# Kernel optimization log

Measured on AMD Instinct MI355X. Metric: run time of the kernel, lower is better.

## Reference

```python
import jax, jax.numpy as jnp
import numpy as np

S_MC = 4      # num_mc_samples
TEMP = 0.1    # soft_sampling temperature


def gcn_conv(x, adj, maskf, W, b):
    # DenseGCNConv: add self loops, sym-normalize, aggregate, linear, mask
    N = adj.shape[-1]
    A = adj + jnp.eye(N, dtype=adj.dtype)
    dis = jnp.clip(A.sum(-1), 1.0, None) ** -0.5
    A = dis[:, :, None] * A * dis[:, None, :]
    out = jnp.einsum('bij,bjf->bif', A, x @ W) + b
    return out * maskf[:, :, None]


def connected_components(adj, mask):
    # min-label propagation; labels in {1..N}, masked nodes -> 0
    B, N, _ = adj.shape
    labels0 = jnp.broadcast_to(jnp.arange(1, N + 1, dtype=jnp.int32), (B, N))
    big = jnp.int32(N + 2)
    adj_b = adj > 0
    def step(labels, _):
        nb = jnp.where(adj_b, labels[:, None, :], big)  # [B,N,N]
        return jnp.minimum(labels, nb.min(-1)), None
    labels, _ = jax.lax.scan(step, labels0, None, length=N)
    return jnp.where(mask, labels, 0)


def setup_inputs() -> dict:
    key = jax.random.key(0)
    ks = jax.random.split(key, 8)
    B, N, Fin, H, K = 512, 64, 128, 256, 32
    x = jax.random.normal(ks[0], (B, N, Fin), jnp.float32)
    lengths = jax.random.randint(ks[1], (B,), N // 2, N + 1)
    mask = jnp.arange(N)[None, :] < lengths[:, None]
    a = jax.random.uniform(ks[2], (B, N, N)) < 0.08
    adj = jnp.triu(a, 1)
    adj = (adj | jnp.swapaxes(adj, 1, 2)).astype(jnp.float32)
    adj = adj * mask[:, :, None] * mask[:, None, :]
    W1 = jax.random.normal(ks[3], (Fin, H), jnp.float32) / np.float32(np.sqrt(Fin))
    b1 = jnp.zeros((H,), jnp.float32)
    W2 = jax.random.normal(ks[4], (H, H), jnp.float32) / np.float32(np.sqrt(H))
    b2 = jnp.zeros((H,), jnp.float32)
    centroids = jax.random.normal(ks[5], (K, H), jnp.float32)
    return {'x': x, 'adj': adj, 'mask': mask, 'W1': W1, 'b1': b1, 'W2': W2, 'b2': b2, 'centroids': centroids}


def reference(x, adj, mask, W1, b1, W2, b2, centroids):
    B, N = mask.shape
    maskf = mask.astype(x.dtype)
    adj = adj * maskf[:, :, None] * maskf[:, None, :]
    # embedding convs
    h = jax.nn.relu(gcn_conv(x, adj, maskf, W1, b1))
    h = jax.nn.relu(gcn_conv(h, adj, maskf, W2, b2))
    # cdist to (detached) centroids, expanded form to avoid [B,N,K,F] blowup
    c = jax.lax.stop_gradient(centroids)
    d2 = (jnp.sum(h * h, -1, keepdims=True) + jnp.sum(c * c, -1)[None, None]
          - 2.0 * jnp.einsum('bnf,kf->bnk', h, c))
    dist = jnp.sqrt(jnp.clip(d2, 1e-12, None))  # [B,N,K]
    # softmin over clusters with temperature
    logits = -dist / TEMP
    probs = jax.nn.softmax(logits, -1)
    logp = jax.nn.log_softmax(logits, -1)
    # Categorical MC sampling via Gumbel-max
    g = jax.random.gumbel(jax.random.key(42), (S_MC,) + logp.shape, logp.dtype)
    concepts = jnp.argmax(logp[None] + g, -1).reshape(S_MC * B, N)  # [SB,N]
    # per-node sampled probability, product over valid nodes per graph (scatter mul)
    probs_r = jnp.tile(probs, (S_MC, 1, 1))
    node_p = jnp.take_along_axis(probs_r, concepts[..., None], -1)[..., 0]
    mask_r = jnp.tile(mask, (S_MC, 1))
    graph_prob = jnp.prod(jnp.where(mask_r, jax.lax.stop_gradient(node_p), 1.0), -1)  # [SB]
    # same-concept restricted adjacency -> connected components (undirected)
    adj_r = jnp.tile(adj, (S_MC, 1, 1))
    same = concepts[:, :, None] == concepts[:, None, :]
    adj_cc = jnp.where(same, adj_r, 0.0)
    adj_cc = jnp.maximum(adj_cc, jnp.swapaxes(adj_cc, 1, 2))
    labels = connected_components(adj_cc, mask_r)  # [SB,N], 0 reserved for masked
    # scatter-mean node embeddings per cluster; drop reserved cluster 0
    P = jax.nn.one_hot(labels, N + 1, dtype=x.dtype) * mask_r[..., None].astype(x.dtype)  # [SB,N,N+1]
    counts = P.sum(1)  # [SB,N+1]
    h_r = jnp.tile(h, (S_MC, 1, 1))
    new_x = (jnp.einsum('bnc,bnf->bcf', P, h_r) / jnp.clip(counts, 1.0, None)[..., None])[:, 1:, :]
    # pooled adjacency S^T A S, binarized
    new_adj = jnp.einsum('bic,bij,bjd->bcd', P, adj_r, P)[:, 1:, 1:]
    new_adj = (new_adj > 0).astype(x.dtype)
    return new_x, new_adj, graph_prob, labels
```

## Files before the change

kernel.cpp:

```cpp
#include <hip/hip_runtime.h>

#define B_    512

static constexpr float TINYF = 1.17549435e-38f;
typedef float fx4  __attribute__((ext_vector_type(4)));
typedef short bf16x8 __attribute__((ext_vector_type(8)));
typedef float f32x4 __attribute__((ext_vector_type(4)));
typedef unsigned short u16x4 __attribute__((ext_vector_type(4)));

__device__ __forceinline__ unsigned tf_bits(unsigned lo) {
  const unsigned ks0 = 0u, ks1 = 42u, ks2 = 0x1BD11BF0u;
  unsigned x0 = 0u + ks0;
  unsigned x1 = lo + ks1;
#define TFR(r) { x0 += x1; x1 = (x1 << r) | (x1 >> (32 - r)); x1 ^= x0; }
  TFR(13) TFR(15) TFR(26) TFR(6)
  x0 += ks1; x1 += ks2 + 1u;
  TFR(17) TFR(29) TFR(16) TFR(24)
  x0 += ks2; x1 += ks0 + 2u;
  TFR(13) TFR(15) TFR(26) TFR(6)
  x0 += ks0; x1 += ks1 + 3u;
  TFR(17) TFR(29) TFR(16) TFR(24)
  x0 += ks1; x1 += ks2 + 4u;
  TFR(13) TFR(15) TFR(26) TFR(6)
  x0 += ks2; x1 += ks0 + 5u;
#undef TFR
  return x0 ^ x1;
}

__device__ __forceinline__ void split3(float v, unsigned& b1, unsigned& b2, unsigned& b3) {
  unsigned u1 = __float_as_uint(v) & 0xFFFF0000u;
  float r1 = v - __uint_as_float(u1);
  unsigned u2 = __float_as_uint(r1) & 0xFFFF0000u;
  float r2 = r1 - __uint_as_float(u2);
  unsigned u3 = __float_as_uint(r2) & 0xFFFF0000u;
  b1 = u1 >> 16; b2 = u2 >> 16; b3 = u3 >> 16;
}

__device__ __forceinline__ unsigned short planeOf(float v, int s) {
  unsigned u1 = __float_as_uint(v) & 0xFFFF0000u;
  if (s == 0) return (unsigned short)(u1 >> 16);
  float r1 = v - __uint_as_float(u1);
  unsigned u2 = __float_as_uint(r1) & 0xFFFF0000u;
  if (s == 1) return (unsigned short)(u2 >> 16);
  float r2 = r1 - __uint_as_float(u2);
  return (unsigned short)((__float_as_uint(r2) & 0xFFFF0000u) >> 16);
}

#define MF6(A0, A1, A2, Bv0, Bv1, Bv2, ACC)                                   \
  ACC = __builtin_amdgcn_mfma_f32_16x16x32_bf16(A0, Bv0, ACC, 0, 0, 0);       \
  ACC = __builtin_amdgcn_mfma_f32_16x16x32_bf16(A0, Bv1, ACC, 0, 0, 0);       \
  ACC = __builtin_amdgcn_mfma_f32_16x16x32_bf16(A1, Bv0, ACC, 0, 0, 0);       \
  ACC = __builtin_amdgcn_mfma_f32_16x16x32_bf16(A0, Bv2, ACC, 0, 0, 0);       \
  ACC = __builtin_amdgcn_mfma_f32_16x16x32_bf16(A1, Bv1, ACC, 0, 0, 0);       \
  ACC = __builtin_amdgcn_mfma_f32_16x16x32_bf16(A2, Bv0, ACC, 0, 0, 0);

__global__ void k_setup(const float* __restrict__ W1, const float* __restrict__ W2,
                        const float* __restrict__ cen,
                        unsigned short* __restrict__ Wg1, unsigned short* __restrict__ Wg2,
                        unsigned short* __restrict__ cen3, float* __restrict__ ccbuf) {
  int bi = blockIdx.x, tid = threadIdx.x;
  if (bi < 144) {
    const float* W; unsigned short* Wg; int nk, s, ks, g;
    if (bi < 48) { W = W1; Wg = Wg1; nk = 4; s = bi >> 4; ks = (bi >> 2) & 3; g = bi & 3; }
    else { int t = bi - 48; W = W2; Wg = Wg2; nk = 8; s = t >> 5; ks = (t >> 2) & 7; g = t & 3; }
    int n = tid;
    bf16x8 hv;
#pragma unroll
    for (int jj = 0; jj < 8; ++jj) {
      float v = W[(size_t)(ks * 32 + g * 8 + jj) * 256 + n];
      hv[jj] = (short)planeOf(v, s);
    }
    *(bf16x8*)&Wg[((((size_t)s * nk + ks) * 4 + g) * 256 + n) * 8] = hv;
  } else if (bi == 144) {
    int k = tid >> 3, l8 = tid & 7;
    float s = 0.0f;
    for (int m = 0; m < 32; ++m) { float v = cen[k * 256 + l8 + 8 * m]; s += v * v; }
#pragma unroll
    for (int d = 1; d < 8; d <<= 1) s += __shfl_xor(s, d, 64);
    if (l8 == 0) ccbuf[k] = s;
  } else {
    int s = bi - 145;
    for (int u = 0; u < 4; ++u) {
      int idx = tid + 256 * u;
      int ks = idx >> 7, c = (idx >> 6) & 1, rem = idx & 63;
      int l15v = rem >> 2, lgv = rem & 3;
      bf16x8 hv;
#pragma unroll
      for (int jj = 0; jj < 8; ++jj)
        hv[jj] = (short)planeOf(cen[(size_t)(16 * c + l15v) * 256 + 32 * ks + 8 * lgv + jj], s);
      *(bf16x8*)&cen3[(size_t)s * 8192 + (size_t)idx * 8] = hv;
    }
  }
}

template<bool SRCL>
__device__ __forceinline__ void layer_core(const float* __restrict__ Aglob,
                                           const float (*hsrc)[260],
                                           float (*hdst)[260],
                                           const unsigned short* __restrict__ Wg, int nk,
                                           const unsigned short* AhP,
                                           const float* biaS, const float* maskS,
                                           char* U, int tid) {
  unsigned short (*Ap)[3][2112] = (unsigned short(*)[3][2112])U;
  unsigned short (*Tbuf)[72]    = (unsigned short(*)[72])U;
  int w = tid >> 6, l = tid & 63;
  int l15 = l & 15, lg = l >> 4;
  int K = nk * 32;
  int srow = tid >> 2, sg = tid & 3;
  const float* sp = SRCL ? (const float*)nullptr : (Aglob + (size_t)srow * K + sg * 8);

  {
    float vv[8];
    if (SRCL) {
      float4 v0 = *(const float4*)&hsrc[srow][sg * 8];
      float4 v1 = *(const float4*)&hsrc[srow][sg * 8 + 4];
      vv[0] = v0.x; vv[1] = v0.y; vv[2] = v0.z; vv[3] = v0.w;
      vv[4] = v1.x; vv[5] = v1.y; vv[6] = v1.z; vv[7] = v1.w;
    } else {
      float4 v0 = *(const float4*)(sp);
      float4 v1 = *(const float4*)(sp + 4);
      vv[0] = v0.x; vv[1] = v0.y; vv[2] = v0.z; vv[3] = v0.w;
      vv[4] = v1.x; vv[5] = v1.y; vv[6] = v1.z; vv[7] = v1.w;
    }
    bf16x8 p1, p2, p3;
#pragma unroll
    for (int jj = 0; jj < 8; ++jj) {
      unsigned h1, h2, h3; split3(vv[jj], h1, h2, h3);
      p1[jj] = (short)h1; p2[jj] = (short)h2; p3[jj] = (short)h3;
    }
    int off = sg * 528 + srow * 8;
    *(bf16x8*)&Ap[0][0][off] = p1;
    *(bf16x8*)&Ap[0][1][off] = p2;
    *(bf16x8*)&Ap[0][2][off] = p3;
  }
  __syncthreads();

  f32x4 acc1[4][4];
#pragma unroll
  for (int q = 0; q < 4; ++q)
#pragma unroll
    for (int c = 0; c < 4; ++c) acc1[q][c] = (f32x4){0.f, 0.f, 0.f, 0.f};

  const size_t wss = (size_t)nk * 8192;

  for (int ks = 0; ks < nk; ++ks) {
    int cur = ks & 1;
    float vv[8];
    bool pf = (ks + 1 < nk);
    if (pf) {
      if (SRCL) {
        float4 v0 = *(const float4*)&hsrc[srow][(ks + 1) * 32 + sg * 8];
        float4 v1 = *(const float4*)&hsrc[srow][(ks + 1) * 32 + sg * 8 + 4];
        vv[0] = v0.x; vv[1] = v0.y; vv[2] = v0.z; vv[3] = v0.w;
        vv[4] = v1.x; vv[5] = v1.y; vv[6] = v1.z; vv[7] = v1.w;
      } else {
        float4 v0 = *(const float4*)(sp + (ks + 1) * 32);
        float4 v1 = *(const float4*)(sp + (ks + 1) * 32 + 4);
        vv[0] = v0.x; vv[1] = v0.y; vv[2] = v0.z; vv[3] = v0.w;
        vv[4] = v1.x; vv[5] = v1.y; vv[6] = v1.z; vv[7] = v1.w;
      }
    }
    bf16x8 af[4][3];
#pragma unroll
    for (int q = 0; q < 4; ++q) {
      int off = lg * 528 + (16 * q + l15) * 8;
#pragma unroll
      for (int s = 0; s < 3; ++s) af[q][s] = *(const bf16x8*)&Ap[cur][s][off];
    }
#pragma unroll
    for (int c = 0; c < 4; ++c) {
      size_t wbase = (((size_t)ks * 4 + lg) * 256 + (64 * w + 16 * c + l15)) * 8;
      bf16x8 b0 = *(const bf16x8*)&Wg[wbase];
      bf16x8 b1 = *(const bf16x8*)&Wg[wbase + wss];
      bf16x8 b2 = *(const bf16x8*)&Wg[wbase + 2 * wss];
#pragma unroll
      for (int q = 0; q < 4; ++q) {
        MF6(af[q][0], af[q][1], af[q][2], b0, b1, b2, acc1[q][c]);
      }
    }
    if (pf) {
      bf16x8 p1, p2, p3;
#pragma unroll
      for (int jj = 0; jj < 8; ++jj) {
        unsigned h1, h2, h3; split3(vv[jj], h1, h2, h3);
        p1[jj] = (short)h1; p2[jj] = (short)h2; p3[jj] = (short)h3;
      }
      int off = sg * 528 + srow * 8;
      *(bf16x8*)&Ap[cur ^ 1][0][off] = p1;
      *(bf16x8*)&Ap[cur ^ 1][1][off] = p2;
      *(bf16x8*)&Ap[cur ^ 1][2][off] = p3;
    }
    __syncthreads();
  }

  f32x4 acc2[4][4];
#pragma unroll
  for (int q = 0; q < 4; ++q)
#pragma unroll
    for (int c = 0; c < 4; ++c) acc2[q][c] = (f32x4){0.f, 0.f, 0.f, 0.f};

#pragma unroll
  for (int sB = 0; sB < 3; ++sB) {
    const int nA = 3 - sB;
    __syncthreads();
#pragma unroll
    for (int q = 0; q < 4; ++q)
#pragma unroll
      for (int c = 0; c < 4; ++c) {
        u16x4 pv;
#pragma unroll
        for (int r = 0; r < 4; ++r) pv[r] = planeOf(acc1[q][c][r], sB);
        *(u16x4*)&Tbuf[64 * w + 16 * c + l15][16 * q + 4 * lg] = pv;
      }
    __syncthreads();
#pragma unroll
    for (int mt = 0; mt < 2; ++mt) {
      bf16x8 bf[4];
#pragma unroll
      for (int c = 0; c < 4; ++c)
        bf[c] = *(const bf16x8*)&Tbuf[64 * w + 16 * c + l15][32 * mt + 8 * lg];
#pragma unroll
      for (int q2 = 0; q2 < 4; ++q2) {
        bf16x8 afr[3];
#pragma unroll
        for (int sA = 0; sA < 3; ++sA)
          if (sA < nA)
            afr[sA] = *(const bf16x8*)&AhP[((((size_t)(sA * 2 + mt) * 4 + q2) * 4 + lg) * 16 + l15) * 8];
#pragma unroll
        for (int c = 0; c < 4; ++c)
#pragma unroll
          for (int sA = 0; sA < 3; ++sA)
            if (sA < nA)
              acc2[q2][c] = __builtin_amdgcn_mfma_f32_16x16x32_bf16(afr[sA], bf[c], acc2[q2][c], 0, 0, 0);
      }
    }
  }

#pragma unroll
  for (int q2 = 0; q2 < 4; ++q2) {
#pragma unroll
    for (int c = 0; c < 4; ++c) {
      int n = 64 * w + 16 * c + l15;
      float bv = biaS[n];
#pragma unroll
      for (int r = 0; r < 4; ++r) {
        int row = 16 * q2 + 4 * lg + r;
        hdst[row][n] = fmaxf((acc2[q2][c][r] + bv) * maskS[row], 0.0f);
      }
    }
  }
}

__global__ __launch_bounds__(256, 1) void k_mega(
    const float* __restrict__ x, const float* __restrict__ adj,
    const void* __restrict__ mp,
    const float* __restrict__ b1v, const float* __restrict__ b2v,
    const unsigned short* __restrict__ Wg1, const unsigned short* __restrict__ Wg2,
    const unsigned short* __restrict__ cen3, const float* __restrict__ ccbuf,
    float* __restrict__ out_newx, float* __restrict__ out_newadj,
    float* __restrict__ out_gp, float* __restrict__ out_lab) {
  __shared__ float hbuf[64][260];
  __shared__ unsigned short AhP[12288];
  __shared__ float maskS[64];
  __shared__ float biaS[256];
  __shared__ unsigned long long nbrS[64];
  __shared__ int concS[4][64];
  __shared__ float ppS[4][64];
  __shared__ float hhp[64][4];
  __shared__ float mxs[64], lgden[64];
  __shared__ int labFS[4][64];
  __shared__ int s_ni, s_nf;
  __shared__ __align__(16) char U[46592];

  int b = blockIdx.x, tid = threadIdx.x;

  {
    float* adjS = (float*)U;
    float (*AhS)[65] = (float(*)[65])(U + 16384);
    float* dis = (float*)(U + 33024);
    if (tid == 0) { s_ni = 0; s_nf = 0; }
    const float* ab = adj + (size_t)b * 4096;
    for (int i = tid; i < 4096; i += 256) adjS[i] = ab[i];
    {
      const unsigned* wp = (const unsigned*)mp;
      int ni = 0, nf = 0;
      for (int i = tid; i < 2048; i += 256) {
        unsigned v = wp[i];
        if (v > 1u) ni = 1;
        if (v != 0u && v != 0x3f800000u) nf = 1;
      }
      if (ni) atomicOr(&s_ni, 1);
      if (nf) atomicOr(&s_nf, 1);
    }
    biaS[tid] = b1v[tid];
    __syncthreads();
    if (tid < 64) {
      float s = 0.0f;
      unsigned long long m = 0ull;
      for (int j = 0; j < 64; ++j) {
        float v = adjS[j * 64 + tid];
        s += (j == tid) ? (v + 1.0f) : v;
        if (v != 0.0f) m |= (1ull << j);
      }
      dis[tid] = 1.0f / sqrtf(fmaxf(s, 1.0f));
      nbrS[tid] = m;
      int fl = s_ni ? (s_nf ? 2 : 1) : 0;
      int i = b * 64 + tid;
      float r;
      if (fl == 0)      r = ((const int*)mp)[i] ? 1.0f : 0.0f;
      else if (fl == 1) r = (((const float*)mp)[i] != 0.0f) ? 1.0f : 0.0f;
      else              r = ((const unsigned char*)mp)[i] ? 1.0f : 0.0f;
      maskS[tid] = r;
    }
    __syncthreads();
    for (int i = tid; i < 4096; i += 256) {
      int r = i >> 6, c = i & 63;
      float a = adjS[i] + ((r == c) ? 1.0f : 0.0f);
      AhS[r][c] = (dis[r] * a) * dis[c];
    }
    __syncthreads();
    for (int ch = tid; ch < 1536; ch += 256) {
      int l15v = ch & 15, lgv = (ch >> 4) & 3, q2 = (ch >> 6) & 3, mt = (ch >> 8) & 1, s = ch >> 9;
      bf16x8 hv;
#pragma unroll
      for (int jj = 0; jj < 8; ++jj)
        hv[jj] = (short)planeOf(AhS[16 * q2 + l15v][32 * mt + 8 * lgv + jj], s);
      *(bf16x8*)&AhP[(size_t)ch * 8] = hv;
    }
    __syncthreads();
  }

  layer_core<false>(x + (size_t)b * 64 * 128, nullptr, hbuf, Wg1, 4, AhP, biaS, maskS, U, tid);
  __syncthreads();
  biaS[tid] = b2v[tid];

  layer_core<true>(nullptr, (const float(*)[260])hbuf, hbuf, Wg2, 8, AhP, biaS, maskS, U, tid);
  __syncthreads();

  {
    float (*Dred)[64][36] = (float(*)[64][36])U;
    float (*lgp)[33] = (float(*)[33])(U + 36864);
    int w = tid >> 6, l = tid & 63, l15 = l & 15, lg = l >> 4;

    {
      int row = tid & 63, qt = tid >> 6;
      float s = 0.0f;
      for (int u = 0; u < 16; ++u) {
        float4 v = *(const float4*)&hbuf[row][qt * 64 + u * 4];
        s += v.x * v.x + v.y * v.y + v.z * v.z + v.w * v.w;
      }
      hhp[row][qt] = s;
    }

    f32x4 acc[4][2];
#pragma unroll
    for (int qt = 0; qt < 4; ++qt)
#pragma unroll
      for (int c = 0; c < 2; ++c) acc[qt][c] = (f32x4){0.f, 0.f, 0.f, 0.f};

#pragma unroll
    for (int ks2 = 0; ks2 < 2; ++ks2) {
      int ks = 2 * w + ks2;
#pragma unroll
      for (int qt = 0; qt < 4; ++qt) {
        int row = 16 * qt + l15;
        float4 v0 = *(const float4*)&hbuf[row][32 * ks + 8 * lg];
        float4 v1 = *(const float4*)&hbuf[row][32 * ks + 8 * lg + 4];
        float vv[8] = {v0.x, v0.y, v0.z, v0.w, v1.x, v1.y, v1.z, v1.w};
        bf16x8 a0, a1, a2;
#pragma unroll
        for (int jj = 0; jj < 8; ++jj) {
          unsigned h1, h2, h3; split3(vv[jj], h1, h2, h3);
          a0[jj] = (short)h1; a1[jj] = (short)h2; a2[jj] = (short)h3;
        }
#pragma unroll
        for (int c = 0; c < 2; ++c) {
          const unsigned short* cb = cen3 + ((size_t)(ks * 2 + c) * 64 + l15 * 4 + lg) * 8;
          bf16x8 b0 = *(const bf16x8*)cb;
          bf16x8 b1 = *(const bf16x8*)(cb + 8192);
          bf16x8 b2 = *(const bf16x8*)(cb + 16384);
          MF6(a0, a1, a2, b0, b1, b2, acc[qt][c]);
        }
      }
    }

#pragma unroll
    for (int qt = 0; qt < 4; ++qt)
#pragma unroll
      for (int c = 0; c < 2; ++c)
#pragma unroll
        for (int r = 0; r < 4; ++r)
          Dred[w][16 * qt + 4 * lg + r][16 * c + l15] = acc[qt][c][r];
    __syncthreads();

    {
      int n = tid >> 2, kq = tid & 3;
      float hh = (hhp[n][0] + hhp[n][1]) + (hhp[n][2] + hhp[n][3]);
#pragma unroll
      for (int j = 0; j < 8; ++j) {
        int k = kq * 8 + j;
        float dot = (Dred[0][n][k] + Dred[1][n][k]) + (Dred[2][n][k] + Dred[3][n][k]);
        float d2 = (hh + ccbuf[k]) - 2.0f * dot;
        lgp[n][k] = -10.0f * sqrtf(fmaxf(d2, 1e-12f));
      }
    }
    __syncthreads();

    if (tid < 64) {
      float mx = -1e30f;
      for (int k = 0; k < 32; ++k) mx = fmaxf(mx, lgp[tid][k]);
      float den = 0.0f;
      for (int k = 0; k < 32; ++k) den += expf(lgp[tid][k] - mx);
      mxs[tid] = mx; lgden[tid] = logf(den);
    }
    __syncthreads();
    for (int p = tid; p < 2048; p += 256) {
      int n = p >> 5, k = p & 31;
      lgp[n][k] = (lgp[n][k] - mxs[n]) - lgden[n];
    }
    __syncthreads();

    int hw = tid >> 5, k = tid & 31;
    for (int pass = 0; pass < 8; ++pass) {
      int n = hw * 8 + pass;
      float lp = lgp[n][k];
#pragma unroll
      for (int s4 = 0; s4 < 4; ++s4) {
        unsigned flat = (unsigned)(s4 * 32768 + b * 64 + n) * 32u + (unsigned)k;
        unsigned bits = tf_bits(flat);
        float fu = __uint_as_float((bits >> 9) | 0x3f800000u) - 1.0f;
        float u = fmaxf(TINYF, fu * (1.0f - TINYF) + TINYF);
        float g = -logf(-logf(u));
        float v = lp + g;
        int bi = k;
#pragma unroll
        for (int d = 1; d < 32; d <<= 1) {
          float ov = __shfl_xor(v, d, 32);
          int oi = __shfl_xor(bi, d, 32);
          if (ov > v || (ov == v && oi < bi)) { v = ov; bi = oi; }
        }
        if (k == 0) {
          concS[s4][n] = bi;
          ppS[s4][n] = expf(lgp[n][bi]);
        }
      }
    }
    __syncthreads();
  }

  {
    unsigned char (*o)[4096] = (unsigned char(*)[4096])U;
    int s = tid >> 6, lane = tid & 63;
    int sbo = s * 512 + b;
    int c0 = concS[s][lane];
    bool mk = maskS[lane] != 0.0f;
    unsigned long long nb = nbrS[lane];
    unsigned long long sm = 0ull;
    {
      unsigned long long t = nb;
      while (t) { int j = __ffsll(t) - 1; if (concS[s][j] == c0) sm |= (1ull << j); t &= t - 1; }
    }
    labFS[s][lane] = lane + 1;
    for (int it = 0; it < 64; ++it) {
      int m = labFS[s][lane];
      unsigned long long t = sm;
      while (t) { int j = __ffsll(t) - 1; m = min(m, labFS[s][j]); t &= t - 1; }
      bool ch = m < labFS[s][lane];
      if (ch) labFS[s][lane] = m;
      if (!__any(ch)) break;
    }
    int lf = mk ? labFS[s][lane] : 0;
    out_lab[(size_t)sbo * 64 + lane] = (float)lf;
    float pv = mk ? ppS[s][lane] : 1.0f;
#pragma unroll
    for (int d = 1; d < 64; d <<= 1) pv *= __shfl_xor(pv, d, 64);
    if (lane == 0) out_gp[sbo] = pv;
    labFS[s][lane] = lf;
    unsigned long long cm = 0ull;
    for (int j = 0; j < 64; ++j)
      if (labFS[s][j] == lane + 1) cm |= (1ull << j);
    {
      unsigned* op = (unsigned*)o[s];
#pragma unroll
      for (int u = 0; u < 16; ++u) op[u * 64 + lane] = 0u;
      int li = lf;
      if (li > 0) {
        unsigned long long t = nb;
        while (t) {
          int j = __ffsll(t) - 1; t &= t - 1;
          int lj = labFS[s][j];
          if (lj > 0) o[s][(li - 1) * 64 + (lj - 1)] = 1;
        }
      }
      float* dA = out_newadj + (size_t)sbo * 4096;
#pragma unroll
      for (int u = 0; u < 16; ++u) {
        int base = u * 256 + lane * 4;
        fx4 v;
        v.x = o[s][base + 0] ? 1.0f : 0.0f;
        v.y = o[s][base + 1] ? 1.0f : 0.0f;
        v.z = o[s][base + 2] ? 1.0f : 0.0f;
        v.w = o[s][base + 3] ? 1.0f : 0.0f;
        __builtin_nontemporal_store(v, (fx4*)&dA[base]);
      }
    }
    float* dX = out_newx + (size_t)sbo * 64 * 256;
    for (int c = 0; c < 64; ++c) {
      unsigned long long m = __shfl(cm, c, 64);
      float4 acc = make_float4(0.f, 0.f, 0.f, 0.f);
      unsigned long long t = m;
      while (t) {
        int j = __ffsll(t) - 1; t &= t - 1;
        float4 v = *(const float4*)&hbuf[j][lane * 4];
        acc.x += v.x; acc.y += v.y; acc.z += v.z; acc.w += v.w;
      }
      int cnt = __popcll(m);
      float cf = (float)(cnt > 0 ? cnt : 1);
      fx4 r;
      r.x = acc.x / cf; r.y = acc.y / cf; r.z = acc.z / cf; r.w = acc.w / cf;
      __builtin_nontemporal_store(r, (fx4*)&dX[(size_t)c * 256 + lane * 4]);
    }
  }
}

extern "C" void kernel_launch(void* const* d_in, const int* in_sizes, int n_in,
                              void* d_out, int out_size, void* d_ws, size_t ws_size,
                              hipStream_t stream) {
  (void)in_sizes; (void)n_in; (void)out_size; (void)ws_size;
  const float* x   = (const float*)d_in[0];
  const float* adj = (const float*)d_in[1];
  const void*  mp  = d_in[2];
  const float* W1  = (const float*)d_in[3];
  const float* b1  = (const float*)d_in[4];
  const float* W2  = (const float*)d_in[5];
  const float* b2  = (const float*)d_in[6];
  const float* cen = (const float*)d_in[7];

  char* ws = (char*)d_ws;
  unsigned short* Wg1  = (unsigned short*)(ws + 0);
  unsigned short* Wg2  = (unsigned short*)(ws + 196608);
  unsigned short* cen3 = (unsigned short*)(ws + 589824);
  float* ccbuf         = (float*)(ws + 638976);

  float* out        = (float*)d_out;
  float* out_newx   = out;
  float* out_newadj = out + 33554432;
  float* out_gp     = out + 41943040;
  float* out_lab    = out + 41945088;

  hipLaunchKernelGGL(k_setup, dim3(148), dim3(256), 0, stream, W1, W2, cen, Wg1, Wg2, cen3, ccbuf);
  hipLaunchKernelGGL(k_mega,  dim3(512), dim3(256), 0, stream, x, adj, mp, b1, b2,
                     Wg1, Wg2, cen3, ccbuf, out_newx, out_newadj, out_gp, out_lab);
}
```

Before: 180.1 us.

## Split mega-kernel into GCN kernel and cdist/sampling/pooling kernel via global buffers

```diff
diff --git a/kernel.cpp b/kernel.cpp
--- a/kernel.cpp
+++ b/kernel.cpp
@@ -7,6 +7,10 @@
 typedef short bf16x8 __attribute__((ext_vector_type(8)));
 typedef float f32x4 __attribute__((ext_vector_type(4)));
 typedef unsigned short u16x4 __attribute__((ext_vector_type(4)));
+
+__device__ __forceinline__ float fmul_s(float a, float b) { float r; asm("v_mul_f32 %0, %1, %2" : "=v"(r) : "v"(a), "v"(b)); return r; }
+__device__ __forceinline__ float fadd_s(float a, float b) { float r; asm("v_add_f32 %0, %1, %2" : "=v"(r) : "v"(a), "v"(b)); return r; }
+__device__ __forceinline__ float fsub_s(float a, float b) { float r; asm("v_sub_f32 %0, %1, %2" : "=v"(r) : "v"(a), "v"(b)); return r; }
 
 __device__ __forceinline__ unsigned tf_bits(unsigned lo) {
   const unsigned ks0 = 0u, ks1 = 42u, ks2 = 0x1BD11BF0u;
@@ -93,35 +97,24 @@
   }
 }
 
-template<bool SRCL>
-__device__ __forceinline__ void layer_core(const float* __restrict__ Aglob,
-                                           const float (*hsrc)[260],
-                                           float (*hdst)[260],
-                                           const unsigned short* __restrict__ Wg, int nk,
+__device__ __forceinline__ void layer_core(const float* __restrict__ A,
+                                           const unsigned short* __restrict__ Wg,
                                            const unsigned short* AhP,
                                            const float* biaS, const float* maskS,
-                                           char* U, int tid) {
+                                           float* __restrict__ out, int nk,
+                                           char* U, int b, int tid) {
   unsigned short (*Ap)[3][2112] = (unsigned short(*)[3][2112])U;
   unsigned short (*Tbuf)[72]    = (unsigned short(*)[72])U;
   int w = tid >> 6, l = tid & 63;
   int l15 = l & 15, lg = l >> 4;
   int K = nk * 32;
   int srow = tid >> 2, sg = tid & 3;
-  const float* sp = SRCL ? (const float*)nullptr : (Aglob + (size_t)srow * K + sg * 8);
+  const float* sp = A + (size_t)srow * K + sg * 8;
 
   {
-    float vv[8];
-    if (SRCL) {
-      float4 v0 = *(const float4*)&hsrc[srow][sg * 8];
-      float4 v1 = *(const float4*)&hsrc[srow][sg * 8 + 4];
-      vv[0] = v0.x; vv[1] = v0.y; vv[2] = v0.z; vv[3] = v0.w;
-      vv[4] = v1.x; vv[5] = v1.y; vv[6] = v1.z; vv[7] = v1.w;
-    } else {
-      float4 v0 = *(const float4*)(sp);
-      float4 v1 = *(const float4*)(sp + 4);
-      vv[0] = v0.x; vv[1] = v0.y; vv[2] = v0.z; vv[3] = v0.w;
-      vv[4] = v1.x; vv[5] = v1.y; vv[6] = v1.z; vv[7] = v1.w;
-    }
+    float4 v0 = *(const float4*)(sp);
+    float4 v1 = *(const float4*)(sp + 4);
+    float vv[8] = {v0.x, v0.y, v0.z, v0.w, v1.x, v1.y, v1.z, v1.w};
     bf16x8 p1, p2, p3;
 #pragma unroll
     for (int jj = 0; jj < 8; ++jj) {
@@ -145,20 +138,11 @@
 
   for (int ks = 0; ks < nk; ++ks) {
     int cur = ks & 1;
-    float vv[8];
+    float4 v0, v1;
     bool pf = (ks + 1 < nk);
     if (pf) {
-      if (SRCL) {
-        float4 v0 = *(const float4*)&hsrc[srow][(ks + 1) * 32 + sg * 8];
-        float4 v1 = *(const float4*)&hsrc[srow][(ks + 1) * 32 + sg * 8 + 4];
-        vv[0] = v0.x; vv[1] = v0.y; vv[2] = v0.z; vv[3] = v0.w;
-        vv[4] = v1.x; vv[5] = v1.y; vv[6] = v1.z; vv[7] = v1.w;
-      } else {
-        float4 v0 = *(const float4*)(sp + (ks + 1) * 32);
-        float4 v1 = *(const float4*)(sp + (ks + 1) * 32 + 4);
-        vv[0] = v0.x; vv[1] = v0.y; vv[2] = v0.z; vv[3] = v0.w;
-        vv[4] = v1.x; vv[5] = v1.y; vv[6] = v1.z; vv[7] = v1.w;
-      }
+      v0 = *(const float4*)(sp + (ks + 1) * 32);
+      v1 = *(const float4*)(sp + (ks + 1) * 32 + 4);
     }
     bf16x8 af[4][3];
 #pragma unroll
@@ -179,6 +163,7 @@
       }
     }
     if (pf) {
+      float vv[8] = {v0.x, v0.y, v0.z, v0.w, v1.x, v1.y, v1.z, v1.w};
       bf16x8 p1, p2, p3;
 #pragma unroll
       for (int jj = 0; jj < 8; ++jj) {
@@ -245,32 +230,25 @@
 #pragma unroll
       for (int r = 0; r < 4; ++r) {
         int row = 16 * q2 + 4 * lg + r;
-        hdst[row][n] = fmaxf((acc2[q2][c][r] + bv) * maskS[row], 0.0f);
-      }
-    }
-  }
-}
-
-__global__ __launch_bounds__(256, 1) void k_mega(
+        float val = (acc2[q2][c][r] + bv) * maskS[row];
+        out[((size_t)b * 64 + row) * 256 + n] = fmaxf(val, 0.0f);
+      }
+    }
+  }
+}
+
+__global__ __launch_bounds__(256, 2) void k_fused(
     const float* __restrict__ x, const float* __restrict__ adj,
     const void* __restrict__ mp,
     const float* __restrict__ b1v, const float* __restrict__ b2v,
     const unsigned short* __restrict__ Wg1, const unsigned short* __restrict__ Wg2,
-    const unsigned short* __restrict__ cen3, const float* __restrict__ ccbuf,
-    float* __restrict__ out_newx, float* __restrict__ out_newadj,
-    float* __restrict__ out_gp, float* __restrict__ out_lab) {
-  __shared__ float hbuf[64][260];
+    unsigned long long* __restrict__ nbr, float* __restrict__ maskf,
+    float* __restrict__ bufA, float* __restrict__ bufB) {
   __shared__ unsigned short AhP[12288];
+  __shared__ float biaS[256];
   __shared__ float maskS[64];
-  __shared__ float biaS[256];
-  __shared__ unsigned long long nbrS[64];
-  __shared__ int concS[4][64];
-  __shared__ float ppS[4][64];
-  __shared__ float hhp[64][4];
-  __shared__ float mxs[64], lgden[64];
-  __shared__ int labFS[4][64];
   __shared__ int s_ni, s_nf;
-  __shared__ __align__(16) char U[46592];
+  __shared__ __align__(16) char U[36864];
 
   int b = blockIdx.x, tid = threadIdx.x;
 
@@ -303,7 +281,7 @@
         if (v != 0.0f) m |= (1ull << j);
       }
       dis[tid] = 1.0f / sqrtf(fmaxf(s, 1.0f));
-      nbrS[tid] = m;
+      nbr[b * 64 + tid] = m;
       int fl = s_ni ? (s_nf ? 2 : 1) : 0;
       int i = b * 64 + tid;
       float r;
@@ -311,6 +289,7 @@
       else if (fl == 1) r = (((const float*)mp)[i] != 0.0f) ? 1.0f : 0.0f;
       else              r = ((const unsigned char*)mp)[i] ? 1.0f : 0.0f;
       maskS[tid] = r;
+      maskf[i] = r;
     }
     __syncthreads();
     for (int i = tid; i < 4096; i += 256) {
@@ -330,96 +309,128 @@
     __syncthreads();
   }
 
-  layer_core<false>(x + (size_t)b * 64 * 128, nullptr, hbuf, Wg1, 4, AhP, biaS, maskS, U, tid);
+  layer_core(x + (size_t)b * 64 * 128, Wg1, AhP, biaS, maskS, bufA, 4, U, b, tid);
   __syncthreads();
   biaS[tid] = b2v[tid];
 
-  layer_core<true>(nullptr, (const float(*)[260])hbuf, hbuf, Wg2, 8, AhP, biaS, maskS, U, tid);
-  __syncthreads();
+  layer_core(bufA + (size_t)b * 64 * 256, Wg2, AhP, biaS, maskS, bufB, 8, U, b, tid);
+}
+
+__global__ __launch_bounds__(256) void k_cdsp(const float* __restrict__ h,
+                                              const unsigned short* __restrict__ cen3,
+                                              const float* __restrict__ ccbuf,
+                                              const float* __restrict__ maskf,
+                                              const unsigned long long* __restrict__ nbr,
+                                              float* __restrict__ out_newx,
+                                              float* __restrict__ out_newadj,
+                                              float* __restrict__ out_gp,
+                                              float* __restrict__ out_lab) {
+  __shared__ float hS[16384];
+  __shared__ float Dred[4][64][36];
+  __shared__ float hhp[64][4];
+  __shared__ float lgp[64][33];
+  __shared__ float mxs[64], lgden[64];
+  __shared__ int concS[4][64];
+  __shared__ float ppS[4][64];
+  __shared__ int labFS[4][64];
+
+  int b = blockIdx.x, tid = threadIdx.x;
+  int w = tid >> 6, l = tid & 63, l15 = l & 15, lg = l >> 4;
+  const float* hb = h + (size_t)b * 16384;
+
+#pragma unroll
+  for (int i = 0; i < 16; ++i) {
+    int g = tid + 256 * i;
+    float4 v = *(const float4*)&hb[(size_t)g * 4];
+    int row = g >> 6;
+    int fb = ((g & 63) * 16) ^ ((row & 7) << 4);
+    *(float4*)((char*)&hS[row * 256] + fb) = v;
+  }
+  __syncthreads();
+
+#define LD4(row, fbyte) (*(const float4*)((const char*)&hS[(row) * 256] + ((fbyte) ^ (((row) & 7) << 4))))
 
   {
-    float (*Dred)[64][36] = (float(*)[64][36])U;
-    float (*lgp)[33] = (float(*)[33])(U + 36864);
-    int w = tid >> 6, l = tid & 63, l15 = l & 15, lg = l >> 4;
-
-    {
-      int row = tid & 63, qt = tid >> 6;
-      float s = 0.0f;
-      for (int u = 0; u < 16; ++u) {
-        float4 v = *(const float4*)&hbuf[row][qt * 64 + u * 4];
-        s += v.x * v.x + v.y * v.y + v.z * v.z + v.w * v.w;
-      }
-      hhp[row][qt] = s;
-    }
-
-    f32x4 acc[4][2];
-#pragma unroll
-    for (int qt = 0; qt < 4; ++qt)
-#pragma unroll
-      for (int c = 0; c < 2; ++c) acc[qt][c] = (f32x4){0.f, 0.f, 0.f, 0.f};
-
-#pragma unroll
-    for (int ks2 = 0; ks2 < 2; ++ks2) {
-      int ks = 2 * w + ks2;
-#pragma unroll
-      for (int qt = 0; qt < 4; ++qt) {
-        int row = 16 * qt + l15;
-        float4 v0 = *(const float4*)&hbuf[row][32 * ks + 8 * lg];
-        float4 v1 = *(const float4*)&hbuf[row][32 * ks + 8 * lg + 4];
-        float vv[8] = {v0.x, v0.y, v0.z, v0.w, v1.x, v1.y, v1.z, v1.w};
-        bf16x8 a0, a1, a2;
-#pragma unroll
-        for (int jj = 0; jj < 8; ++jj) {
-          unsigned h1, h2, h3; split3(vv[jj], h1, h2, h3);
-          a0[jj] = (short)h1; a1[jj] = (short)h2; a2[jj] = (short)h3;
-        }
-#pragma unroll
-        for (int c = 0; c < 2; ++c) {
-          const unsigned short* cb = cen3 + ((size_t)(ks * 2 + c) * 64 + l15 * 4 + lg) * 8;
-          bf16x8 b0 = *(const bf16x8*)cb;
-          bf16x8 b1 = *(const bf16x8*)(cb + 8192);
-          bf16x8 b2 = *(const bf16x8*)(cb + 16384);
-          MF6(a0, a1, a2, b0, b1, b2, acc[qt][c]);
-        }
-      }
-    }
-
-#pragma unroll
-    for (int qt = 0; qt < 4; ++qt)
-#pragma unroll
-      for (int c = 0; c < 2; ++c)
-#pragma unroll
-        for (int r = 0; r < 4; ++r)
-          Dred[w][16 * qt + 4 * lg + r][16 * c + l15] = acc[qt][c][r];
-    __syncthreads();
-
-    {
-      int n = tid >> 2, kq = tid & 3;
-      float hh = (hhp[n][0] + hhp[n][1]) + (hhp[n][2] + hhp[n][3]);
-#pragma unroll
-      for (int j = 0; j < 8; ++j) {
-        int k = kq * 8 + j;
-        float dot = (Dred[0][n][k] + Dred[1][n][k]) + (Dred[2][n][k] + Dred[3][n][k]);
-        float d2 = (hh + ccbuf[k]) - 2.0f * dot;
-        lgp[n][k] = -10.0f * sqrtf(fmaxf(d2, 1e-12f));
-      }
-    }
-    __syncthreads();
-
-    if (tid < 64) {
-      float mx = -1e30f;
-      for (int k = 0; k < 32; ++k) mx = fmaxf(mx, lgp[tid][k]);
-      float den = 0.0f;
-      for (int k = 0; k < 32; ++k) den += expf(lgp[tid][k] - mx);
-      mxs[tid] = mx; lgden[tid] = logf(den);
-    }
-    __syncthreads();
-    for (int p = tid; p < 2048; p += 256) {
-      int n = p >> 5, k = p & 31;
-      lgp[n][k] = (lgp[n][k] - mxs[n]) - lgden[n];
-    }
-    __syncthreads();
-
+    int row = tid & 63, qt = tid >> 6;
+    float s = 0.0f;
+    for (int u = 0; u < 16; ++u) {
+      float4 v = LD4(row, qt * 256 + u * 16);
+      float t = fadd_s(fadd_s(fadd_s(fmul_s(v.x, v.x), fmul_s(v.y, v.y)), fmul_s(v.z, v.z)), fmul_s(v.w, v.w));
+      s = fadd_s(s, t);
+    }
+    hhp[row][qt] = s;
+  }
+
+  f32x4 acc[4][2];
+#pragma unroll
+  for (int qt = 0; qt < 4; ++qt)
+#pragma unroll
+    for (int c = 0; c < 2; ++c) acc[qt][c] = (f32x4){0.f, 0.f, 0.f, 0.f};
+
+#pragma unroll
+  for (int ks2 = 0; ks2 < 2; ++ks2) {
+    int ks = 2 * w + ks2;
+#pragma unroll
+    for (int qt = 0; qt < 4; ++qt) {
+      int row = 16 * qt + l15;
+      int fb = (32 * ks + 8 * lg) * 4;
+      float4 v0 = LD4(row, fb);
+      float4 v1 = LD4(row, fb + 16);
+      float vv[8] = {v0.x, v0.y, v0.z, v0.w, v1.x, v1.y, v1.z, v1.w};
+      bf16x8 a0, a1, a2;
+#pragma unroll
+      for (int jj = 0; jj < 8; ++jj) {
+        unsigned h1, h2, h3; split3(vv[jj], h1, h2, h3);
+        a0[jj] = (short)h1; a1[jj] = (short)h2; a2[jj] = (short)h3;
+      }
+#pragma unroll
+      for (int c = 0; c < 2; ++c) {
+        const unsigned short* cb = cen3 + ((size_t)(ks * 2 + c) * 64 + l15 * 4 + lg) * 8;
+        bf16x8 b0 = *(const bf16x8*)cb;
+        bf16x8 b1 = *(const bf16x8*)(cb + 8192);
+        bf16x8 b2 = *(const bf16x8*)(cb + 16384);
+        MF6(a0, a1, a2, b0, b1, b2, acc[qt][c]);
+      }
+    }
+  }
+
+#pragma unroll
+  for (int qt = 0; qt < 4; ++qt)
+#pragma unroll
+    for (int c = 0; c < 2; ++c)
+#pragma unroll
+      for (int r = 0; r < 4; ++r)
+        Dred[w][16 * qt + 4 * lg + r][16 * c + l15] = acc[qt][c][r];
+  __syncthreads();
+
+  {
+    int n = tid >> 2, kq = tid & 3;
+    float hh = (hhp[n][0] + hhp[n][1]) + (hhp[n][2] + hhp[n][3]);
+#pragma unroll
+    for (int j = 0; j < 8; ++j) {
+      int k = kq * 8 + j;
+      float dot = (Dred[0][n][k] + Dred[1][n][k]) + (Dred[2][n][k] + Dred[3][n][k]);
+      float d2 = fsub_s(fadd_s(hh, ccbuf[k]), fmul_s(2.0f, dot));
+      lgp[n][k] = -10.0f * sqrtf(fmaxf(d2, 1e-12f));
+    }
+  }
+  __syncthreads();
+
+  if (tid < 64) {
+    float mx = -1e30f;
+    for (int k = 0; k < 32; ++k) mx = fmaxf(mx, lgp[tid][k]);
+    float den = 0.0f;
+    for (int k = 0; k < 32; ++k) den += expf(lgp[tid][k] - mx);
+    mxs[tid] = mx; lgden[tid] = logf(den);
+  }
+  __syncthreads();
+  for (int p = tid; p < 2048; p += 256) {
+    int n = p >> 5, k = p & 31;
+    lgp[n][k] = (lgp[n][k] - mxs[n]) - lgden[n];
+  }
+  __syncthreads();
+
+  {
     int hw = tid >> 5, k = tid & 31;
     for (int pass = 0; pass < 8; ++pass) {
       int n = hw * 8 + pass;
@@ -429,7 +440,7 @@
         unsigned flat = (unsigned)(s4 * 32768 + b * 64 + n) * 32u + (unsigned)k;
         unsigned bits = tf_bits(flat);
         float fu = __uint_as_float((bits >> 9) | 0x3f800000u) - 1.0f;
-        float u = fmaxf(TINYF, fu * (1.0f - TINYF) + TINYF);
+        float u = fmaxf(TINYF, fadd_s(fmul_s(fu, 1.0f - TINYF), TINYF));
         float g = -logf(-logf(u));
         float v = lp + g;
         int bi = k;
@@ -445,16 +456,16 @@
         }
       }
     }
-    __syncthreads();
-  }
+  }
+  __syncthreads();
 
   {
-    unsigned char (*o)[4096] = (unsigned char(*)[4096])U;
-    int s = tid >> 6, lane = tid & 63;
+    unsigned char (*o)[4096] = (unsigned char(*)[4096])Dred;
+    int s = w, lane = l;
     int sbo = s * 512 + b;
     int c0 = concS[s][lane];
-    bool mk = maskS[lane] != 0.0f;
-    unsigned long long nb = nbrS[lane];
+    bool mk = maskf[b * 64 + lane] != 0.0f;
+    unsigned long long nb = nbr[b * 64 + lane];
     unsigned long long sm = 0ull;
     {
       unsigned long long t = nb;
@@ -483,13 +494,12 @@
       unsigned* op = (unsigned*)o[s];
 #pragma unroll
       for (int u = 0; u < 16; ++u) op[u * 64 + lane] = 0u;
-      int li = lf;
-      if (li > 0) {
+      if (lf > 0) {
         unsigned long long t = nb;
         while (t) {
           int j = __ffsll(t) - 1; t &= t - 1;
           int lj = labFS[s][j];
-          if (lj > 0) o[s][(li - 1) * 64 + (lj - 1)] = 1;
+          if (lj > 0) o[s][(lf - 1) * 64 + (lj - 1)] = 1;
         }
       }
       float* dA = out_newadj + (size_t)sbo * 4096;
@@ -504,23 +514,24 @@
         __builtin_nontemporal_store(v, (fx4*)&dA[base]);
       }
     }
-    float* dX = out_newx + (size_t)sbo * 64 * 256;
+    float* dX = out_newx + (size_t)sbo * 16384;
     for (int c = 0; c < 64; ++c) {
       unsigned long long m = __shfl(cm, c, 64);
-      float4 acc = make_float4(0.f, 0.f, 0.f, 0.f);
+      float4 acc4 = make_float4(0.f, 0.f, 0.f, 0.f);
       unsigned long long t = m;
       while (t) {
         int j = __ffsll(t) - 1; t &= t - 1;
-        float4 v = *(const float4*)&hbuf[j][lane * 4];
-        acc.x += v.x; acc.y += v.y; acc.z += v.z; acc.w += v.w;
+        float4 v = LD4(j, lane * 16);
+        acc4.x += v.x; acc4.y += v.y; acc4.z += v.z; acc4.w += v.w;
       }
       int cnt = __popcll(m);
       float cf = (float)(cnt > 0 ? cnt : 1);
       fx4 r;
-      r.x = acc.x / cf; r.y = acc.y / cf; r.z = acc.z / cf; r.w = acc.w / cf;
+      r.x = acc4.x / cf; r.y = acc4.y / cf; r.z = acc4.z / cf; r.w = acc4.w / cf;
       __builtin_nontemporal_store(r, (fx4*)&dX[(size_t)c * 256 + lane * 4]);
     }
   }
+#undef LD4
 }
 
 extern "C" void kernel_launch(void* const* d_in, const int* in_sizes, int n_in,
@@ -541,6 +552,10 @@
   unsigned short* Wg2  = (unsigned short*)(ws + 196608);
   unsigned short* cen3 = (unsigned short*)(ws + 589824);
   float* ccbuf         = (float*)(ws + 638976);
+  unsigned long long* nbr = (unsigned long long*)(ws + 655360);
+  float* maskf         = (float*)(ws + 917504);
+  float* bufA          = (float*)(ws + 2097152);
+  float* bufB          = (float*)(ws + 37748736);
 
   float* out        = (float*)d_out;
   float* out_newx   = out;
@@ -549,6 +564,8 @@
   float* out_lab    = out + 41945088;
 
   hipLaunchKernelGGL(k_setup, dim3(148), dim3(256), 0, stream, W1, W2, cen, Wg1, Wg2, cen3, ccbuf);
-  hipLaunchKernelGGL(k_mega,  dim3(512), dim3(256), 0, stream, x, adj, mp, b1, b2,
-                     Wg1, Wg2, cen3, ccbuf, out_newx, out_newadj, out_gp, out_lab);
-}
+  hipLaunchKernelGGL(k_fused, dim3(512), dim3(256), 0, stream, x, adj, mp, b1, b2,
+                     Wg1, Wg2, nbr, maskf, bufA, bufB);
+  hipLaunchKernelGGL(k_cdsp,  dim3(512), dim3(256), 0, stream, bufB, cen3, ccbuf, maskf, nbr,
+                     out_newx, out_newadj, out_gp, out_lab);
+}
```

New measurement: 170.3 us. 5.4% less time.
